# Kernel optimization log

Hardware: AMD Instinct MI355X
Metric: run time of the kernel (lower is better)

## Reference

```python
import jax, jax.numpy as jnp
import numpy as np

B, CI, CO, H, W, M1, M2 = 4, 64, 64, 256, 256, 16, 16


def setup_inputs() -> dict:
    key = jax.random.key(0)
    k0, k1, k2, k3, k4 = jax.random.split(key, 5)
    scale = 1.0 / (CI * CO)
    x = jax.random.normal(k0, (B, CI, H, W), dtype=jnp.float32)
    # torch.rand -> uniform [0,1), scaled; real/imag parts of complex weights
    w1r = scale * jax.random.uniform(k1, (CO, CI, M1, M2), dtype=jnp.float32)
    w1i = scale * jax.random.uniform(k2, (CO, CI, M1, M2), dtype=jnp.float32)
    w2r = scale * jax.random.uniform(k3, (CO, CI, M1, M2), dtype=jnp.float32)
    w2i = scale * jax.random.uniform(k4, (CO, CI, M1, M2), dtype=jnp.float32)
    return {"x": x, "w1r": w1r, "w1i": w1i, "w2r": w2r, "w2i": w2i}


def reference(x, w1r, w1i, w2r, w2i):
    b, ci, h, w = x.shape
    co, _, m1, m2 = w1r.shape
    wf = w // 2 + 1  # rfft width
    x_ft = jnp.fft.rfft2(x)                       # [b, ci, h, wf] complex
    xs = x_ft[:, :, :m1, :m2]                     # low-frequency slice
    w1 = w1r + 1j * w1i
    w2 = w2r + 1j * w2i
    o1 = jnp.einsum('bixy,ioxy->boxy', xs, w1)    # [b, co, m1, m2]
    o2 = jnp.einsum('bixy,ioxy->boxy', xs, w2)    # same slice, per original code
    out_ft = jnp.zeros((b, co, h, wf), dtype=x_ft.dtype)
    out_ft = out_ft.at[:, :, :m1, :m2].set(o1)
    out_ft = out_ft.at[:, :, h - m1:, :m2].set(o2)
    return jnp.fft.irfft2(out_ft, s=(h, w))
```

## Files before the change

kernel.cpp:

```cpp
#include <hip/hip_runtime.h>

#define NB 4
#define NCI 64
#define NCO 64
#define PLANE 65536

#define OF_XS_RE 0
#define OF_XS_IM (OF_XS_RE + PLANE)

#define XEOFF(w) ((w)*260)
#define XOOFF(w) (16*260 + 8 + (w)*260)

#define TPF 6.2831853071795864769f

__global__ __launch_bounds__(1024, 4) void k12_dft(const float* __restrict__ x,
                                                   float* __restrict__ ws) {
  __shared__ float bufA[8336], bufB[8336];
  __shared__ float cst[256], snt[256];
  __shared__ float2 s2[1024];
  const int t = threadIdx.x;
  const int img = blockIdx.x;

  if (t < 256) {
    float sv_, cv_;
    sincosf(TPF * (float)t * (1.0f/256.0f), &sv_, &cv_);
    cst[t] = cv_;  snt[t] = sv_;
  }

  const int sl = t & 3, row = t >> 2;
  const int wq = t & 3, p = (t >> 2) & 1;
  const int kg = (t >> 3) & 1, tr = t >> 4;
  int kyv[4];
#pragma unroll
  for (int j = 0; j < 4; ++j) kyv[j] = p + 8*kg + 2*j;

  const float* xb = x + (size_t)img * 65536;

  float4 lo0 = *(const float4*)(xb + row*256 + sl*4);
  float4 hi0 = *(const float4*)(xb + row*256 + 128 + sl*4);
  float4 lo1 = *(const float4*)(xb + row*256 + 16 + sl*4);
  float4 hi1 = *(const float4*)(xb + row*256 + 144 + sl*4);

  __syncthreads();

  float cd[4], sd[4];
#pragma unroll
  for (int j = 0; j < 4; ++j) { cd[j] = cst[kyv[j]]; sd[j] = snt[kyv[j]]; }

  float ar[4][4], ai[4][4];
#pragma unroll
  for (int j = 0; j < 4; ++j)
#pragma unroll
    for (int r = 0; r < 4; ++r) { ar[j][r] = 0.f; ai[j][r] = 0.f; }

  bufA[XEOFF(sl*4+0) + row] = lo0.x + hi0.x;
  bufA[XEOFF(sl*4+1) + row] = lo0.y + hi0.y;
  bufA[XEOFF(sl*4+2) + row] = lo0.z + hi0.z;
  bufA[XEOFF(sl*4+3) + row] = lo0.w + hi0.w;
  bufA[XOOFF(sl*4+0) + row] = lo0.x - hi0.x;
  bufA[XOOFF(sl*4+1) + row] = lo0.y - hi0.y;
  bufA[XOOFF(sl*4+2) + row] = lo0.z - hi0.z;
  bufA[XOOFF(sl*4+3) + row] = lo0.w - hi0.w;
  __syncthreads();

  const int pofs = p ? (16*260 + 8) : 0;

  for (int c = 0; c < 8; ++c) {
    float* cur = (c & 1) ? bufB : bufA;
    float* nxt = (c & 1) ? bufA : bufB;
    if (c < 6) {
      const int w0n = (c+2) * 16;
      if (c & 1) {
        lo1 = *(const float4*)(xb + row*256 + w0n + sl*4);
        hi1 = *(const float4*)(xb + row*256 + w0n + 128 + sl*4);
      } else {
        lo0 = *(const float4*)(xb + row*256 + w0n + sl*4);
        hi0 = *(const float4*)(xb + row*256 + w0n + 128 + sl*4);
      }
    }
    float cc[4], sv[4];
#pragma unroll
    for (int j = 0; j < 4; ++j) {
      const int m = (kyv[j] * (c*16 + wq*4)) & 255;
      cc[j] = cst[m];
      sv[j] = snt[m];
    }
    const float* rp = cur + pofs;
#pragma unroll
    for (int i = 0; i < 4; ++i) {
      const int wl = wq*4 + i;
      const float4 xs4 = *(const float4*)&rp[wl*260 + tr*4];
#pragma unroll
      for (int j = 0; j < 4; ++j) {
        ar[j][0] += xs4.x * cc[j];  ai[j][0] -= xs4.x * sv[j];
        ar[j][1] += xs4.y * cc[j];  ai[j][1] -= xs4.y * sv[j];
        ar[j][2] += xs4.z * cc[j];  ai[j][2] -= xs4.z * sv[j];
        ar[j][3] += xs4.w * cc[j];  ai[j][3] -= xs4.w * sv[j];
        const float nc = cc[j]*cd[j] - sv[j]*sd[j];
        const float ns = sv[j]*cd[j] + cc[j]*sd[j];
        cc[j] = nc; sv[j] = ns;
      }
    }
    if (c < 7) {
      if (c & 1) {
        nxt[XEOFF(sl*4+0) + row] = lo0.x + hi0.x;
        nxt[XEOFF(sl*4+1) + row] = lo0.y + hi0.y;
        nxt[XEOFF(sl*4+2) + row] = lo0.z + hi0.z;
        nxt[XEOFF(sl*4+3) + row] = lo0.w + hi0.w;
        nxt[XOOFF(sl*4+0) + row] = lo0.x - hi0.x;
        nxt[XOOFF(sl*4+1) + row] = lo0.y - hi0.y;
        nxt[XOOFF(sl*4+2) + row] = lo0.z - hi0.z;
        nxt[XOOFF(sl*4+3) + row] = lo0.w - hi0.w;
      } else {
        nxt[XEOFF(sl*4+0) + row] = lo1.x + hi1.x;
        nxt[XEOFF(sl*4+1) + row] = lo1.y + hi1.y;
        nxt[XEOFF(sl*4+2) + row] = lo1.z + hi1.z;
        nxt[XEOFF(sl*4+3) + row] = lo1.w + hi1.w;
        nxt[XOOFF(sl*4+0) + row] = lo1.x - hi1.x;
        nxt[XOOFF(sl*4+1) + row] = lo1.y - hi1.y;
        nxt[XOOFF(sl*4+2) + row] = lo1.z - hi1.z;
        nxt[XOOFF(sl*4+3) + row] = lo1.w - hi1.w;
      }
    }
    __syncthreads();
  }

#pragma unroll
  for (int j = 0; j < 4; ++j)
#pragma unroll
    for (int r = 0; r < 4; ++r) {
      ar[j][r] += __shfl_xor(ar[j][r], 1);
      ar[j][r] += __shfl_xor(ar[j][r], 2);
      ai[j][r] += __shfl_xor(ai[j][r], 1);
      ai[j][r] += __shfl_xor(ai[j][r], 2);
    }
  if (wq == 0) {
#pragma unroll
    for (int j = 0; j < 4; ++j) {
      const int ky = kyv[j];
      float4 sr; sr.x = ar[j][0]; sr.y = ar[j][1]; sr.z = ar[j][2]; sr.w = ar[j][3];
      float4 si; si.x = ai[j][0]; si.y = ai[j][1]; si.z = ai[j][2]; si.w = ai[j][3];
      *(float4*)&bufA[XEOFF(ky) + tr*4] = sr;
      *(float4*)&bufA[XOOFF(ky) + tr*4] = si;
    }
  }
  __syncthreads();

  const int ky2 = t & 15, kx = (t >> 4) & 15, hh = t >> 8;
  const float sg = (kx & 1) ? -1.f : 1.f;
  const float cdk = cst[kx], sdk = snt[kx];
  const int m0 = (kx * hh * 32) & 255;
  float cR = cst[m0], sR = snt[m0];
  float arr = 0.f, aii = 0.f;
  const int be = XEOFF(ky2) + hh*32;
  const int bo = XOOFF(ky2) + hh*32;
#pragma unroll 4
  for (int hq = 0; hq < 8; ++hq) {
    const float4 xrL = *(const float4*)&bufA[be + hq*4];
    const float4 xrH = *(const float4*)&bufA[be + 128 + hq*4];
    const float4 xiL = *(const float4*)&bufA[bo + hq*4];
    const float4 xiH = *(const float4*)&bufA[bo + 128 + hq*4];
    {
      const float xr = xrL.x + sg*xrH.x, xi = xiL.x + sg*xiH.x;
      arr += xr*cR + xi*sR;  aii += xi*cR - xr*sR;
      const float nc = cR*cdk - sR*sdk, ns = sR*cdk + cR*sdk; cR = nc; sR = ns;
    }
    {
      const float xr = xrL.y + sg*xrH.y, xi = xiL.y + sg*xiH.y;
      arr += xr*cR + xi*sR;  aii += xi*cR - xr*sR;
      const float nc = cR*cdk - sR*sdk, ns = sR*cdk + cR*sdk; cR = nc; sR = ns;
    }
    {
      const float xr = xrL.z + sg*xrH.z, xi = xiL.z + sg*xiH.z;
      arr += xr*cR + xi*sR;  aii += xi*cR - xr*sR;
      const float nc = cR*cdk - sR*sdk, ns = sR*cdk + cR*sdk; cR = nc; sR = ns;
    }
    {
      const float xr = xrL.w + sg*xrH.w, xi = xiL.w + sg*xiH.w;
      arr += xr*cR + xi*sR;  aii += xi*cR - xr*sR;
      const float nc = cR*cdk - sR*sdk, ns = sR*cdk + cR*sdk; cR = nc; sR = ns;
    }
  }
  s2[t].x = arr; s2[t].y = aii;
  __syncthreads();
  if (t < 256) {
    float xre = s2[t].x + s2[t+256].x + s2[t+512].x + s2[t+768].x;
    float xim = s2[t].y + s2[t+256].y + s2[t+512].y + s2[t+768].y;
    ws[OF_XS_RE + img*256 + t] = xre;
    ws[OF_XS_IM + img*256 + t] = xim;
  }
}

__global__ __launch_bounds__(256) void k345_idft(const float* __restrict__ w1r,
    const float* __restrict__ w1i, const float* __restrict__ w2r,
    const float* __restrict__ w2i, const float* __restrict__ ws,
    float* __restrict__ out) {
  __shared__ __align__(16) float o1r[256], o1i[256], o2r[256], o2i[256];
  __shared__ float cst[256], snt[256];
  __shared__ __align__(16) float Sr[128][20], Si[128][20];
  const int t   = threadIdx.x;
  const int bo  = blockIdx.x >> 1;
  const int hcc = blockIdx.x & 1;

  {
    float sv_, cv_;
    sincosf(TPF * (float)t * (1.0f/256.0f), &sv_, &cv_);
    cst[t] = cv_;  snt[t] = sv_;
  }

  {
    const int b = bo >> 6, o = bo & 63;
    const float* xsr = ws + OF_XS_RE;
    const float* xsi = ws + OF_XS_IM;
    float a1r=0.f, a1i=0.f, a2r=0.f, a2i=0.f;
#pragma unroll 4
    for (int i = 0; i < NCI; ++i) {
      const int xi_ = ((b*NCI + i) << 8) + t;
      const float xr = xsr[xi_];
      const float xi = xsi[xi_];
      const int wi = ((i*NCO + o) << 8) + t;
      const float pw = w1r[wi], q = w1i[wi], u = w2r[wi], v = w2i[wi];
      a1r += xr*pw - xi*q;
      a1i += xr*q + xi*pw;
      a2r += xr*u - xi*v;
      a2i += xr*v + xi*u;
    }
    o1r[t] = a1r;
    o1i[t] = a1i;
    o2r[t] = a2r;
    o2i[t] = a2i;
  }
  __syncthreads();

  {
    const int hl = t >> 2, kq = t & 3;
    const int h  = hcc*64 + hl;
    const float chh = cst[h], shh = snt[h];
    float c1 = 1.f, s1 = 0.f;
    const int m2i = (240 * h) & 255;
    float cB = cst[m2i], sB = snt[m2i];
    float4 srE = {0,0,0,0}, siE = {0,0,0,0};
    float4 srO = {0,0,0,0}, siO = {0,0,0,0};
#pragma unroll
    for (int j = 0; j < 16; ++j) {
      const float4 r1 = *(const float4*)&o1r[j*16 + kq*4];
      const float4 i1 = *(const float4*)&o1i[j*16 + kq*4];
      const float4 r2 = *(const float4*)&o2r[j*16 + kq*4];
      const float4 i2 = *(const float4*)&o2i[j*16 + kq*4];
      float4& sr = (j & 1) ? srO : srE;
      float4& si = (j & 1) ? siO : siE;
      sr.x += r1.x*c1 - i1.x*s1 + r2.x*cB - i2.x*sB;
      si.x += r1.x*s1 + i1.x*c1 + r2.x*sB + i2.x*cB;
      sr.y += r1.y*c1 - i1.y*s1 + r2.y*cB - i2.y*sB;
      si.y += r1.y*s1 + i1.y*c1 + r2.y*sB + i2.y*cB;
      sr.z += r1.z*c1 - i1.z*s1 + r2.z*cB - i2.z*sB;
      si.z += r1.z*s1 + i1.z*c1 + r2.z*sB + i2.z*cB;
      sr.w += r1.w*c1 - i1.w*s1 + r2.w*cB - i2.w*sB;
      si.w += r1.w*s1 + i1.w*c1 + r2.w*sB + i2.w*cB;
      const float n1c = c1*chh - s1*shh, n1s = s1*chh + c1*shh;
      const float n2c = cB*chh - sB*shh, n2s = sB*chh + cB*shh;
      c1 = n1c; s1 = n1s; cB = n2c; sB = n2s;
    }
    float4 sp, sm;
    sp.x = srE.x + srO.x; sp.y = srE.y + srO.y; sp.z = srE.z + srO.z; sp.w = srE.w + srO.w;
    sm.x = srE.x - srO.x; sm.y = srE.y - srO.y; sm.z = srE.z - srO.z; sm.w = srE.w - srO.w;
    *(float4*)&Sr[hl][kq*4]      = sp;
    *(float4*)&Sr[hl+64][kq*4]   = sm;
    sp.x = siE.x + siO.x; sp.y = siE.y + siO.y; sp.z = siE.z + siO.z; sp.w = siE.w + siO.w;
    sm.x = siE.x - siO.x; sm.y = siE.y - siO.y; sm.z = siE.z - siO.z; sm.w = siE.w - siO.w;
    *(float4*)&Si[hl][kq*4]      = sp;
    *(float4*)&Si[hl+64][kq*4]   = sm;
  }
  __syncthreads();

  const int wl = t & 31;
  float c[15], s[15], c2[15], s2[15];
#pragma unroll
  for (int k = 0; k < 15; ++k) {
    const int mi = ((k+1) * wl) & 255;
    c[k] = cst[mi];
    s[k] = snt[mi];
  }
  {
    const float R = 0.70710678118654752f;
#pragma unroll
    for (int k = 0; k < 15; ++k) {
      const int r8 = (k + 1) & 7;
      switch (r8) {
        case 0: c2[k] =  c[k];            s2[k] =  s[k];            break;
        case 1: c2[k] = (c[k]-s[k])*R;    s2[k] = (s[k]+c[k])*R;    break;
        case 2: c2[k] = -s[k];            s2[k] =  c[k];            break;
        case 3: c2[k] = -(c[k]+s[k])*R;   s2[k] = (c[k]-s[k])*R;    break;
        case 4: c2[k] = -c[k];            s2[k] = -s[k];            break;
        case 5: c2[k] = (s[k]-c[k])*R;    s2[k] = -(c[k]+s[k])*R;   break;
        case 6: c2[k] =  s[k];            s2[k] = -c[k];            break;
        default:c2[k] = (c[k]+s[k])*R;    s2[k] = (s[k]-c[k])*R;    break;
      }
    }
  }

  const int half = (t >> 5) & 1;
  const int wv = t >> 6;
  const float scale = 2.0f / 65536.0f;
  const size_t base256 = (size_t)bo*256 + hcc*64;
#pragma unroll 2
  for (int pr = 0; pr < 16; ++pr) {
    const int lr = wv*32 + pr*2 + half;
    const float4 a0 = *(const float4*)&Sr[lr][0];
    const float4 a1 = *(const float4*)&Sr[lr][4];
    const float4 a2 = *(const float4*)&Sr[lr][8];
    const float4 a3 = *(const float4*)&Sr[lr][12];
    const float4 b0 = *(const float4*)&Si[lr][0];
    const float4 b1 = *(const float4*)&Si[lr][4];
    const float4 b2 = *(const float4*)&Si[lr][8];
    const float4 b3 = *(const float4*)&Si[lr][12];
    const float re[16] = {a0.x,a0.y,a0.z,a0.w, a1.x,a1.y,a1.z,a1.w,
                          a2.x,a2.y,a2.z,a2.w, a3.x,a3.y,a3.z,a3.w};
    const float im[16] = {b0.x,b0.y,b0.z,b0.w, b1.x,b1.y,b1.z,b1.w,
                          b2.x,b2.y,b2.z,b2.w, b3.x,b3.y,b3.z,b3.w};
    const int grow = (lr & 63) + ((lr >> 6) << 7);
    const size_t ob = (base256 + grow) * 256;

#pragma unroll
    for (int g = 0; g < 2; ++g) {
      const float* cc = g ? c2 : c;
      const float* ss = g ? s2 : s;
      float PA = 0.5f * re[0];
      float PB = 0.f, PC = 0.f, PD = 0.f, QB = 0.f, QD = 0.f;
#pragma unroll
      for (int k = 0; k < 15; ++k) {
        const int ky = k + 1;
        const float R = re[ky], I = im[ky];
        const int cls = ky & 3;
        if (cls == 0)      PA += R*cc[k] - I*ss[k];
        else if (cls == 1) { PB += R*cc[k] - I*ss[k];  QB += R*ss[k] + I*cc[k]; }
        else if (cls == 2) PC += R*cc[k] - I*ss[k];
        else               { PD += R*cc[k] - I*ss[k];  QD += R*ss[k] + I*cc[k]; }
      }
      const float T1 = PA + PC, T2 = PB + PD;
      const float T3 = PA - PC, T4 = QB - QD;
      const int cb = wl + g*32;
      out[ob + cb]       = (T1 + T2) * scale;
      out[ob + cb + 64]  = (T3 - T4) * scale;
      out[ob + cb + 128] = (T1 - T2) * scale;
      out[ob + cb + 192] = (T3 + T4) * scale;
    }
  }
}

extern "C" void kernel_launch(void* const* d_in, const int* in_sizes, int n_in,
                              void* d_out, int out_size, void* d_ws, size_t ws_size,
                              hipStream_t stream) {
  const float* x   = (const float*)d_in[0];
  const float* w1r = (const float*)d_in[1];
  const float* w1i = (const float*)d_in[2];
  const float* w2r = (const float*)d_in[3];
  const float* w2i = (const float*)d_in[4];
  float* out = (float*)d_out;
  float* ws  = (float*)d_ws;

  hipLaunchKernelGGL(k12_dft,   dim3(256), dim3(1024), 0, stream, x, ws);
  hipLaunchKernelGGL(k345_idft, dim3(512), dim3(256),  0, stream,
                     w1r, w1i, w2r, w2i, ws, out);
}
```

Measured before the change: 53.31 us.

## Merge h-halves into one 512-thread block and split channel reduction across threads

The inverse-DFT kernel now uses one 512-thread block per (batch, out-channel) pair instead of two 256-thread blocks that each handled half of the rows. This removes the duplicated per-block work: the 64-channel mode mixing, which read all the weights, was previously computed twice. The channel sum is split into two halves of 32 across thread groups and combined through shared memory, with the Sr/Si buffers reused as scratch. The cost is an extra reduction pass and barrier, larger shared memory per block, and half as many blocks.

Result: faster. 49.78 us (-6.6%).

```diff
diff --git a/kernel.cpp b/kernel.cpp
--- a/kernel.cpp
+++ b/kernel.cpp
@@ -191,50 +191,63 @@
   }
 }
 
-__global__ __launch_bounds__(256) void k345_idft(const float* __restrict__ w1r,
+__global__ __launch_bounds__(512, 2) void k345_idft(const float* __restrict__ w1r,
     const float* __restrict__ w1i, const float* __restrict__ w2r,
     const float* __restrict__ w2i, const float* __restrict__ ws,
     float* __restrict__ out) {
   __shared__ __align__(16) float o1r[256], o1i[256], o2r[256], o2i[256];
   __shared__ float cst[256], snt[256];
-  __shared__ __align__(16) float Sr[128][20], Si[128][20];
-  const int t   = threadIdx.x;
-  const int bo  = blockIdx.x >> 1;
-  const int hcc = blockIdx.x & 1;
-
-  {
+  __shared__ __align__(16) float Sr[256][20], Si[256][20];
+  const int t  = threadIdx.x;
+  const int bo = blockIdx.x;
+
+  if (t < 256) {
     float sv_, cv_;
     sincosf(TPF * (float)t * (1.0f/256.0f), &sv_, &cv_);
     cst[t] = cv_;  snt[t] = sv_;
   }
 
   {
+    const int m = t & 255, ih = t >> 8;
     const int b = bo >> 6, o = bo & 63;
     const float* xsr = ws + OF_XS_RE;
     const float* xsi = ws + OF_XS_IM;
     float a1r=0.f, a1i=0.f, a2r=0.f, a2i=0.f;
 #pragma unroll 4
-    for (int i = 0; i < NCI; ++i) {
-      const int xi_ = ((b*NCI + i) << 8) + t;
+    for (int ii = 0; ii < 32; ++ii) {
+      const int i = ih*32 + ii;
+      const int xi_ = ((b*NCI + i) << 8) + m;
       const float xr = xsr[xi_];
       const float xi = xsi[xi_];
-      const int wi = ((i*NCO + o) << 8) + t;
+      const int wi = ((i*NCO + o) << 8) + m;
       const float pw = w1r[wi], q = w1i[wi], u = w2r[wi], v = w2i[wi];
       a1r += xr*pw - xi*q;
       a1i += xr*q + xi*pw;
       a2r += xr*u - xi*v;
       a2i += xr*v + xi*u;
     }
-    o1r[t] = a1r;
-    o1i[t] = a1i;
-    o2r[t] = a2r;
-    o2i[t] = a2i;
+    float4* pm1 = (float4*)&Sr[0][0];
+    float4* pm2 = (float4*)&Si[0][0];
+    float4 v1; v1.x = a1r; v1.y = a1i; v1.z = 0.f; v1.w = 0.f;
+    float4 v2; v2.x = a2r; v2.y = a2i; v2.z = 0.f; v2.w = 0.f;
+    pm1[t] = v1;
+    pm2[t] = v2;
+  }
+  __syncthreads();
+  if (t < 256) {
+    const float4* pm1 = (const float4*)&Sr[0][0];
+    const float4* pm2 = (const float4*)&Si[0][0];
+    const float4 a = pm1[t], b4 = pm1[t + 256];
+    const float4 c4 = pm2[t], d4 = pm2[t + 256];
+    o1r[t] = a.x + b4.x;
+    o1i[t] = a.y + b4.y;
+    o2r[t] = c4.x + d4.x;
+    o2i[t] = c4.y + d4.y;
   }
   __syncthreads();
 
   {
-    const int hl = t >> 2, kq = t & 3;
-    const int h  = hcc*64 + hl;
+    const int h = t >> 2, kq = t & 3;
     const float chh = cst[h], shh = snt[h];
     float c1 = 1.f, s1 = 0.f;
     const int m2i = (240 * h) & 255;
@@ -264,12 +277,12 @@
     float4 sp, sm;
     sp.x = srE.x + srO.x; sp.y = srE.y + srO.y; sp.z = srE.z + srO.z; sp.w = srE.w + srO.w;
     sm.x = srE.x - srO.x; sm.y = srE.y - srO.y; sm.z = srE.z - srO.z; sm.w = srE.w - srO.w;
-    *(float4*)&Sr[hl][kq*4]      = sp;
-    *(float4*)&Sr[hl+64][kq*4]   = sm;
+    *(float4*)&Sr[h][kq*4]       = sp;
+    *(float4*)&Sr[h+128][kq*4]   = sm;
     sp.x = siE.x + siO.x; sp.y = siE.y + siO.y; sp.z = siE.z + siO.z; sp.w = siE.w + siO.w;
     sm.x = siE.x - siO.x; sm.y = siE.y - siO.y; sm.z = siE.z - siO.z; sm.w = siE.w - siO.w;
-    *(float4*)&Si[hl][kq*4]      = sp;
-    *(float4*)&Si[hl+64][kq*4]   = sm;
+    *(float4*)&Si[h][kq*4]       = sp;
+    *(float4*)&Si[h+128][kq*4]   = sm;
   }
   __syncthreads();
 
@@ -302,7 +315,7 @@
   const int half = (t >> 5) & 1;
   const int wv = t >> 6;
   const float scale = 2.0f / 65536.0f;
-  const size_t base256 = (size_t)bo*256 + hcc*64;
+  const size_t base256 = (size_t)bo * 256;
 #pragma unroll 2
   for (int pr = 0; pr < 16; ++pr) {
     const int lr = wv*32 + pr*2 + half;
@@ -318,8 +331,7 @@
                           a2.x,a2.y,a2.z,a2.w, a3.x,a3.y,a3.z,a3.w};
     const float im[16] = {b0.x,b0.y,b0.z,b0.w, b1.x,b1.y,b1.z,b1.w,
                           b2.x,b2.y,b2.z,b2.w, b3.x,b3.y,b3.z,b3.w};
-    const int grow = (lr & 63) + ((lr >> 6) << 7);
-    const size_t ob = (base256 + grow) * 256;
+    const size_t ob = (base256 + lr) * 256;
 
 #pragma unroll
     for (int g = 0; g < 2; ++g) {
@@ -360,6 +372,6 @@
   float* ws  = (float*)d_ws;
 
   hipLaunchKernelGGL(k12_dft,   dim3(256), dim3(1024), 0, stream, x, ws);
-  hipLaunchKernelGGL(k345_idft, dim3(512), dim3(256),  0, stream,
+  hipLaunchKernelGGL(k345_idft, dim3(256), dim3(512),  0, stream,
                      w1r, w1i, w2r, w2i, ws, out);
 }
```
